# Kernel optimization log

Hardware: AMD Instinct MI355X
Metric: run time of the kernel (lower is better)

Reference implementation:

```python
import jax, jax.numpy as jnp
import numpy as np

B, S, D_IN, E, H = 4, 2048, 1024, 1024, 16
HD = E // H  # 64


def setup_inputs() -> dict:
    key = jax.random.key(0)
    k1, k2, k3, k4, k5 = jax.random.split(key, 5)
    sc_in = 1.0 / np.sqrt(D_IN)
    sc_e = 1.0 / np.sqrt(E)
    return {
        "x": jax.random.normal(k1, (B, S, D_IN), dtype=jnp.float32),
        "w_qkv": jax.random.uniform(k2, (D_IN, 3 * E), dtype=jnp.float32, minval=-sc_in, maxval=sc_in),
        "b_qkv": jax.random.uniform(k3, (3 * E,), dtype=jnp.float32, minval=-sc_in, maxval=sc_in),
        "w_o": jax.random.uniform(k4, (E, E), dtype=jnp.float32, minval=-sc_e, maxval=sc_e),
        "b_o": jax.random.uniform(k5, (E,), dtype=jnp.float32, minval=-sc_e, maxval=sc_e),
    }


def reference(x, w_qkv, b_qkv, w_o, b_o):
    b, s, _ = x.shape
    qkv = x @ w_qkv + b_qkv                          # [B,S,3E]
    qkv = qkv.reshape(b, s, H, 3 * HD)               # [B,S,H,3*HD]
    qkv = qkv.transpose(0, 2, 1, 3)                  # [B,H,S,3*HD]
    q, k, v = jnp.split(qkv, 3, axis=-1)             # each [B,H,S,HD]
    scale = 1.0 / jnp.sqrt(jnp.asarray(HD, dtype=q.dtype))
    logits = jnp.einsum("bhqd,bhkd->bhqk", q, k) * scale
    attn = jax.nn.softmax(logits, axis=-1)
    vals = jnp.einsum("bhqk,bhkd->bhqd", attn, v)    # [B,H,S,HD]
    vals = vals.transpose(0, 2, 1, 3).reshape(b, s, E)
    return vals @ w_o + b_o
```

## Files before the change

### kernel.cpp

```cpp
#include <hip/hip_runtime.h>

typedef __attribute__((ext_vector_type(8))) short bf16x8;
typedef __attribute__((ext_vector_type(4))) float f32x4;
typedef __attribute__((ext_vector_type(16))) float f32x16;
typedef __attribute__((ext_vector_type(4))) unsigned short u16x4;

#define DEV static __device__ __forceinline__

constexpr int Bn = 4, Seq = 2048, DIN = 1024, E = 1024, H = 16, HD = 64;
constexpr int Mrows = Bn * Seq;
constexpr int N3 = 3 * E;

DEV unsigned short f2bf(float f) {
  union { float f; unsigned u; } v; v.f = f;
  return (unsigned short)((v.u + 0x7FFFu + ((v.u >> 16) & 1u)) >> 16);
}

typedef const __attribute__((address_space(1))) unsigned int* gas_p;
typedef __attribute__((address_space(3))) unsigned int* las_p;

DEV void gload_lds16(const void* g, void* l) {
  __builtin_amdgcn_global_load_lds((gas_p)g, (las_p)l, 16, 0, 0);
}

DEV unsigned cvtpk_bf16(float lo, float hi) {
  unsigned r;
  asm("v_cvt_pk_bf16_f32 %0, %1, %2" : "=v"(r) : "v"(lo), "v"(hi));
  return r;
}
DEV float exp2fast(float x) {
  float r;
  asm("v_exp_f32 %0, %1" : "=v"(r) : "v"(x));
  return r;
}
DEV unsigned shx32(unsigned v) { return (unsigned)__shfl_xor((int)v, 32, 64); }
DEV bf16x8 pack4(unsigned w0, unsigned w1, unsigned w2, unsigned w3) {
  union { unsigned u[4]; bf16x8 b; } cv;
  cv.u[0] = w0; cv.u[1] = w1; cv.u[2] = w2; cv.u[3] = w3;
  return cv.b;
}

__global__ void cast_f32_bf16(const float* __restrict__ in,
                              unsigned short* __restrict__ out) {
  size_t i = ((size_t)blockIdx.x * 256 + threadIdx.x) * 8;
  float4 a = *(const float4*)(in + i);
  float4 b = *(const float4*)(in + i + 4);
  union { unsigned short us[8]; bf16x8 v; } r;
  r.us[0] = f2bf(a.x); r.us[1] = f2bf(a.y); r.us[2] = f2bf(a.z); r.us[3] = f2bf(a.w);
  r.us[4] = f2bf(b.x); r.us[5] = f2bf(b.y); r.us[6] = f2bf(b.z); r.us[7] = f2bf(b.w);
  *(bf16x8*)(out + i) = r.v;
}

__global__ void tcast(const float* __restrict__ in, unsigned short* __restrict__ out,
                      int K, int N) {
  __shared__ float tile[64][65];
  int n0 = blockIdx.x * 64, k0 = blockIdx.y * 64;
  int tx = threadIdx.x & 63, ty = threadIdx.x >> 6;
#pragma unroll
  for (int i = 0; i < 64; i += 4)
    tile[ty + i][tx] = in[(size_t)(k0 + ty + i) * N + n0 + tx];
  __syncthreads();
#pragma unroll
  for (int i = 0; i < 64; i += 4)
    out[(size_t)(n0 + ty + i) * K + k0 + tx] = f2bf(tile[tx][ty + i]);
}

template <int EPI, int VOUT>
__global__ __launch_bounds__(256) void gemm_bt(
    const unsigned short* __restrict__ A, const unsigned short* __restrict__ Bt,
    const float* __restrict__ bias, void* __restrict__ Cout,
    unsigned short* __restrict__ vt, int N, int K) {
  constexpr int BM = 128, BN = 128, BK = 32;
  __shared__ alignas(16) unsigned short As[BM * BK];
  __shared__ alignas(16) unsigned short Bs[BN * BK];
  const int tid = threadIdx.x;
  const int wave = tid >> 6, lane = tid & 63;
  const int wr = wave >> 1, wc = wave & 1;
  const int llo = lane & 15, lhi = lane >> 4;
  const int bm = blockIdx.y * BM, bn = blockIdx.x * BN;

  f32x4 acc[4][4] = {};

  for (int kt = 0; kt < K; kt += BK) {
#pragma unroll
    for (int i = 0; i < 2; ++i) {
      int chunk = i * 4 + wave;
      int e = (chunk * 64 + lane) * 8;
      int row = e >> 5, col = e & 31;
      gload_lds16(A + (size_t)(bm + row) * K + kt + col, (char*)As + chunk * 1024);
      gload_lds16(Bt + (size_t)(bn + row) * K + kt + col, (char*)Bs + chunk * 1024);
    }
    __syncthreads();

    bf16x8 af[4], bfr[4];
#pragma unroll
    for (int mt = 0; mt < 4; ++mt)
      af[mt] = *(const bf16x8*)&As[(wr * 64 + mt * 16 + llo) * BK + lhi * 8];
#pragma unroll
    for (int nt = 0; nt < 4; ++nt)
      bfr[nt] = *(const bf16x8*)&Bs[(wc * 64 + nt * 16 + llo) * BK + lhi * 8];
#pragma unroll
    for (int mt = 0; mt < 4; ++mt)
#pragma unroll
      for (int nt = 0; nt < 4; ++nt)
        acc[mt][nt] =
            __builtin_amdgcn_mfma_f32_16x16x32_bf16(af[mt], bfr[nt], acc[mt][nt], 0, 0, 0);
    __syncthreads();
  }

#pragma unroll
  for (int nt = 0; nt < 4; ++nt) {
    int n = bn + wc * 64 + nt * 16 + llo;
    float bv = bias[n];
    if constexpr (VOUT == 1) {
      int h = n / 192, inner = n % 192;
      if (inner < 128) {
        int col = h * 128 + inner;
#pragma unroll
        for (int mt = 0; mt < 4; ++mt)
#pragma unroll
          for (int r = 0; r < 4; ++r) {
            int m = bm + wr * 64 + mt * 16 + lhi * 4 + r;
            ((unsigned short*)Cout)[(size_t)m * 2048 + col] = f2bf(acc[mt][nt][r] + bv);
          }
      } else {
        int d = inner - 128;
#pragma unroll
        for (int mt = 0; mt < 4; ++mt) {
          int m = bm + wr * 64 + mt * 16 + lhi * 4;
          int b = m >> 11, s = m & 2047;
          u16x4 pk;
#pragma unroll
          for (int r = 0; r < 4; ++r) pk[r] = f2bf(acc[mt][nt][r] + bv);
          *(u16x4*)&vt[(size_t)((b * 16 + h) * 64 + d) * Seq + s] = pk;
        }
      }
    } else {
#pragma unroll
      for (int mt = 0; mt < 4; ++mt) {
#pragma unroll
        for (int r = 0; r < 4; ++r) {
          int m = bm + wr * 64 + mt * 16 + lhi * 4 + r;
          float v = acc[mt][nt][r] + bv;
          if constexpr (EPI == 0)
            ((unsigned short*)Cout)[(size_t)m * N + n] = f2bf(v);
          else
            ((float*)Cout)[(size_t)m * N + n] = v;
        }
      }
    }
  }
}

__global__ __launch_bounds__(256) void attn(const unsigned short* __restrict__ qk,
                                            const unsigned short* __restrict__ vt,
                                            unsigned short* __restrict__ O) {
  constexpr int KB = 64, NT = Seq / KB;
  constexpr float SCL = 0.18033688011112042f;
  __shared__ alignas(16) unsigned short Ks[2][64 * 64];
  __shared__ alignas(16) unsigned short Vs[2][64 * 64];
  __shared__ float rbc[4][32];

  const int bh = blockIdx.y, b = bh >> 4, h = bh & 15;
  const int q0 = blockIdx.x * 128;
  const int tid = threadIdx.x, wq = tid >> 6, lane = tid & 63;
  const int lq = lane & 31, hi = lane >> 5;

  const unsigned short* qbase = qk + (size_t)(b * Seq) * 2048 + h * 128;
  const unsigned short* kbase = qbase + 64;
  const unsigned short* vtb = vt + (size_t)bh * 64 * Seq;

  bf16x8 qf[4];
  {
    const unsigned short* qrow = qbase + (size_t)(q0 + wq * 32 + lq) * 2048 + hi * 8;
#pragma unroll
    for (int ds = 0; ds < 4; ++ds) qf[ds] = *(const bf16x8*)(qrow + ds * 16);
  }

  float m = -1e30f, l = 0.f;
  f32x16 oacc[2] = {};

  const int srow = lane >> 3;
  const int scol = ((lane & 7) ^ srow) * 8;

#define STAGE(t, bb)                                                         \
  {                                                                          \
    int kv0 = (t) * KB;                                                      \
    _Pragma("unroll") for (int i = 0; i < 2; ++i) {                          \
      int chunk = i * 4 + wq;                                                \
      int row = chunk * 8 + srow;                                            \
      gload_lds16(kbase + (size_t)(kv0 + row) * 2048 + scol,                 \
                  (char*)&Ks[bb][0] + chunk * 1024);                         \
      gload_lds16(vtb + (size_t)row * Seq + kv0 + scol,                      \
                  (char*)&Vs[bb][0] + chunk * 1024);                         \
    }                                                                        \
  }

#define MKFRAG(dst, s, base)                                                  \
  {                                                                           \
    unsigned a0 = cvtpk_bf16(s[base + 0], s[base + 1]);                       \
    unsigned a1 = cvtpk_bf16(s[base + 2], s[base + 3]);                       \
    unsigned b0 = cvtpk_bf16(s[base + 4], s[base + 5]);                       \
    unsigned b1 = cvtpk_bf16(s[base + 6], s[base + 7]);                       \
    unsigned oa0 = shx32(a0), oa1 = shx32(a1), ob0 = shx32(b0), ob1 = shx32(b1); \
    dst = pack4(hi ? ob0 : a0, hi ? ob1 : a1, hi ? b0 : oa0, hi ? b1 : oa1);  \
  }

  STAGE(0, 0);
  asm volatile("s_waitcnt vmcnt(0)" ::: "memory");
  __syncthreads();

  for (int t = 0; t < NT; ++t) {
    const int bb = t & 1;
    if (t + 1 < NT) STAGE(t + 1, bb ^ 1);

    f32x16 sa0 = {}, sa1 = {};
#pragma unroll
    for (int ds = 0; ds < 4; ++ds) {
      const int ch = 2 * ds + hi;
      bf16x8 k0 = *(const bf16x8*)&Ks[bb][lq * 64 + ((ch ^ (lq & 7)) << 3)];
      bf16x8 k1 = *(const bf16x8*)&Ks[bb][(32 + lq) * 64 + ((ch ^ (lq & 7)) << 3)];
      sa0 = __builtin_amdgcn_mfma_f32_32x32x16_bf16(k0, qf[ds], sa0, 0, 0, 0);
      sa1 = __builtin_amdgcn_mfma_f32_32x32x16_bf16(k1, qf[ds], sa1, 0, 0, 0);
    }

    float tmx[16];
#pragma unroll
    for (int i = 0; i < 16; ++i) tmx[i] = fmaxf(sa0[i], sa1[i]);
#pragma unroll
    for (int st = 8; st > 0; st >>= 1)
#pragma unroll
      for (int i = 0; i < st; ++i) tmx[i] = fmaxf(tmx[i], tmx[i + st]);
    float pmax = tmx[0];
    pmax = fmaxf(pmax, __shfl_xor(pmax, 32, 64));

    float mnew = fmaxf(m, pmax);
    float rfac = exp2fast((m - mnew) * SCL);
    m = mnew;
    float nmc = -m * SCL;

#pragma unroll
    for (int i = 0; i < 16; ++i) sa0[i] = exp2fast(fmaf(sa0[i], SCL, nmc));
#pragma unroll
    for (int i = 0; i < 16; ++i) sa1[i] = exp2fast(fmaf(sa1[i], SCL, nmc));

    float ts[16];
#pragma unroll
    for (int i = 0; i < 16; ++i) ts[i] = sa0[i] + sa1[i];
#pragma unroll
    for (int st = 8; st > 0; st >>= 1)
#pragma unroll
      for (int i = 0; i < st; ++i) ts[i] += ts[i + st];
    float psum = ts[0];
    psum += __shfl_xor(psum, 32, 64);
    l = l * rfac + psum;

    bf16x8 pav[4];
    MKFRAG(pav[0], sa0, 0);
    MKFRAG(pav[1], sa0, 8);
    MKFRAG(pav[2], sa1, 0);
    MKFRAG(pav[3], sa1, 8);

    if (hi == 0) rbc[wq][lq] = rfac;
    f32x4 rf[4];
#pragma unroll
    for (int g = 0; g < 4; ++g) rf[g] = *(const f32x4*)&rbc[wq][g * 8 + hi * 4];
#pragma unroll
    for (int i = 0; i < 16; ++i) {
      float r = rf[i >> 2][i & 3];
      oacc[0][i] *= r;
      oacc[1][i] *= r;
    }

#pragma unroll
    for (int ks = 0; ks < 4; ++ks) {
      const int ch = 2 * ks + hi;
      bf16x8 v0 = *(const bf16x8*)&Vs[bb][lq * 64 + ((ch ^ (lq & 7)) << 3)];
      bf16x8 v1 = *(const bf16x8*)&Vs[bb][(32 + lq) * 64 + ((ch ^ (lq & 7)) << 3)];
      oacc[0] = __builtin_amdgcn_mfma_f32_32x32x16_bf16(pav[ks], v0, oacc[0], 0, 0, 0);
      oacc[1] = __builtin_amdgcn_mfma_f32_32x32x16_bf16(pav[ks], v1, oacc[1], 0, 0, 0);
    }

    asm volatile("s_waitcnt vmcnt(0)" ::: "memory");
    __syncthreads();
  }
#undef STAGE
#undef MKFRAG

  if (hi == 0) rbc[wq][lq] = 1.0f / l;
  f32x4 lf[4];
#pragma unroll
  for (int g = 0; g < 4; ++g) lf[g] = *(const f32x4*)&rbc[wq][g * 8 + hi * 4];
  unsigned short* ob = O + (size_t)(b * Seq + q0 + wq * 32) * E + h * 64 + lq;
#pragma unroll
  for (int db = 0; db < 2; ++db)
#pragma unroll
    for (int i = 0; i < 16; ++i) {
      int ql = (i & 3) + 8 * (i >> 2) + 4 * hi;
      ob[(size_t)ql * E + db * 32] = f2bf(oacc[db][i] * lf[i >> 2][i & 3]);
    }
}

extern "C" void kernel_launch(void* const* d_in, const int* in_sizes, int n_in,
                              void* d_out, int out_size, void* d_ws, size_t ws_size,
                              hipStream_t stream) {
  const float* x = (const float*)d_in[0];
  const float* w_qkv = (const float*)d_in[1];
  const float* b_qkv = (const float*)d_in[2];
  const float* w_o = (const float*)d_in[3];
  const float* b_o = (const float*)d_in[4];
  float* out = (float*)d_out;
  char* ws = (char*)d_ws;

  unsigned short* xb  = (unsigned short*)(ws + 0);
  unsigned short* wqt = (unsigned short*)(ws + 16777216);
  unsigned short* wot = (unsigned short*)(ws + 23068672);
  unsigned short* qkb = (unsigned short*)(ws + 25165824);
  unsigned short* vtb = (unsigned short*)(ws + 58720256);
  unsigned short* atO = (unsigned short*)(ws + 75497472);

  cast_f32_bf16<<<4096, 256, 0, stream>>>(x, xb);
  tcast<<<dim3(48, 16), 256, 0, stream>>>(w_qkv, wqt, DIN, N3);
  tcast<<<dim3(16, 16), 256, 0, stream>>>(w_o, wot, E, E);
  gemm_bt<0, 1><<<dim3(N3 / 128, Mrows / 128), 256, 0, stream>>>(xb, wqt, b_qkv, qkb, vtb, N3, DIN);
  attn<<<dim3(Seq / 128, Bn * H), 256, 0, stream>>>(qkb, vtb, atO);
  gemm_bt<1, 0><<<dim3(E / 128, Mrows / 128), 256, 0, stream>>>(atO, wot, b_o, out, nullptr, E, E);
}
```

Measured before the change: 330.6 us.

## Replace GEMM with 256-row double-buffered XOR-swizzled LDS tiles and 512 threads

Replaces the 128x128x32 GEMM with a 256xBN x64 tile kernel using 8 waves, double-buffered LDS staging via global_load_lds, and an XOR swizzle on LDS columns to avoid bank conflicts. The QKV projection uses BN=192, so each column tile lines up with one head's q/k/v span, and the output projection uses BN=128. The grid is transposed so blockIdx.x walks M. The aim is more data reuse per tile and overlap of global loads with MFMA work. In exchange, register and LDS pressure rise, which may limit occupancy.

Measured after the change: 307.3 us. 1.08x faster.

```diff
diff --git a/kernel.cpp b/kernel.cpp
--- a/kernel.cpp
+++ b/kernel.cpp
@@ -65,69 +65,102 @@
     out[(size_t)(n0 + ty + i) * K + k0 + tx] = f2bf(tile[tx][ty + i]);
 }
 
-template <int EPI, int VOUT>
-__global__ __launch_bounds__(256) void gemm_bt(
+template <int BN, int EPI, int VOUT>
+__global__ __launch_bounds__(512, 2) void gemm256(
     const unsigned short* __restrict__ A, const unsigned short* __restrict__ Bt,
     const float* __restrict__ bias, void* __restrict__ Cout,
     unsigned short* __restrict__ vt, int N, int K) {
-  constexpr int BM = 128, BN = 128, BK = 32;
-  __shared__ alignas(16) unsigned short As[BM * BK];
-  __shared__ alignas(16) unsigned short Bs[BN * BK];
+  constexpr int BM = 256, BK = 64;
+  constexpr int NSPAN = BN / 4;
+  constexpr int NF = NSPAN / 16;
+  constexpr int AC = BM * BK / 8;
+  constexpr int BC = BN * BK / 8;
+  __shared__ alignas(16) unsigned short As[2][BM * BK];
+  __shared__ alignas(16) unsigned short Bs[2][BN * BK];
+
   const int tid = threadIdx.x;
   const int wave = tid >> 6, lane = tid & 63;
-  const int wr = wave >> 1, wc = wave & 1;
+  const int wr = wave >> 2, wc = wave & 3;
   const int llo = lane & 15, lhi = lane >> 4;
-  const int bm = blockIdx.y * BM, bn = blockIdx.x * BN;
-
-  f32x4 acc[4][4] = {};
-
-  for (int kt = 0; kt < K; kt += BK) {
-#pragma unroll
-    for (int i = 0; i < 2; ++i) {
-      int chunk = i * 4 + wave;
-      int e = (chunk * 64 + lane) * 8;
-      int row = e >> 5, col = e & 31;
-      gload_lds16(A + (size_t)(bm + row) * K + kt + col, (char*)As + chunk * 1024);
-      gload_lds16(Bt + (size_t)(bn + row) * K + kt + col, (char*)Bs + chunk * 1024);
-    }
-    __syncthreads();
-
-    bf16x8 af[4], bfr[4];
-#pragma unroll
-    for (int mt = 0; mt < 4; ++mt)
-      af[mt] = *(const bf16x8*)&As[(wr * 64 + mt * 16 + llo) * BK + lhi * 8];
-#pragma unroll
-    for (int nt = 0; nt < 4; ++nt)
-      bfr[nt] = *(const bf16x8*)&Bs[(wc * 64 + nt * 16 + llo) * BK + lhi * 8];
-#pragma unroll
-    for (int mt = 0; mt < 4; ++mt)
-#pragma unroll
-      for (int nt = 0; nt < 4; ++nt)
-        acc[mt][nt] =
-            __builtin_amdgcn_mfma_f32_16x16x32_bf16(af[mt], bfr[nt], acc[mt][nt], 0, 0, 0);
-    __syncthreads();
-  }
-
-#pragma unroll
-  for (int nt = 0; nt < 4; ++nt) {
-    int n = bn + wc * 64 + nt * 16 + llo;
+  const int bm = blockIdx.x * BM, bn = blockIdx.y * BN;
+
+  f32x4 acc[8][NF] = {};
+
+#define GSTAGE(kt, bufi)                                                      \
+  {                                                                           \
+    _Pragma("unroll") for (int i = 0; i < AC / 512; ++i) {                    \
+      int c = i * 512 + tid;                                                  \
+      int row = c >> 3, cs = c & 7;                                           \
+      int col = ((cs ^ (row & 7)) << 3);                                      \
+      gload_lds16(A + (size_t)(bm + row) * K + (kt) + col,                    \
+                  (char*)&As[bufi][0] + c * 16);                              \
+    }                                                                         \
+    _Pragma("unroll") for (int i = 0; i < BC / 512; ++i) {                    \
+      int c = i * 512 + tid;                                                  \
+      int row = c >> 3, cs = c & 7;                                           \
+      int col = ((cs ^ (row & 7)) << 3);                                      \
+      gload_lds16(Bt + (size_t)(bn + row) * K + (kt) + col,                   \
+                  (char*)&Bs[bufi][0] + c * 16);                              \
+    }                                                                         \
+  }
+
+  const int NT = K / BK;
+  GSTAGE(0, 0);
+  asm volatile("s_waitcnt vmcnt(0)" ::: "memory");
+  __syncthreads();
+
+  for (int t = 0; t < NT; ++t) {
+    const int buf = t & 1;
+    if (t + 1 < NT) GSTAGE((t + 1) * BK, buf ^ 1);
+
+#pragma unroll
+    for (int kh = 0; kh < 2; ++kh) {
+      bf16x8 af[8], bfv[NF];
+#pragma unroll
+      for (int mt = 0; mt < 8; ++mt) {
+        int row = wr * 128 + mt * 16 + llo;
+        af[mt] = *(const bf16x8*)&As[buf][row * 64 + (((kh * 4 + lhi) ^ (row & 7)) << 3)];
+      }
+#pragma unroll
+      for (int nt = 0; nt < NF; ++nt) {
+        int row = wc * NSPAN + nt * 16 + llo;
+        bfv[nt] = *(const bf16x8*)&Bs[buf][row * 64 + (((kh * 4 + lhi) ^ (row & 7)) << 3)];
+      }
+#pragma unroll
+      for (int mt = 0; mt < 8; ++mt)
+#pragma unroll
+        for (int nt = 0; nt < NF; ++nt)
+          acc[mt][nt] =
+              __builtin_amdgcn_mfma_f32_16x16x32_bf16(af[mt], bfv[nt], acc[mt][nt], 0, 0, 0);
+    }
+
+    if (t + 1 < NT) {
+      asm volatile("s_waitcnt vmcnt(0)" ::: "memory");
+      __syncthreads();
+    }
+  }
+#undef GSTAGE
+
+#pragma unroll
+  for (int nt = 0; nt < NF; ++nt) {
+    int n = bn + wc * NSPAN + nt * 16 + llo;
     float bv = bias[n];
     if constexpr (VOUT == 1) {
       int h = n / 192, inner = n % 192;
       if (inner < 128) {
         int col = h * 128 + inner;
 #pragma unroll
-        for (int mt = 0; mt < 4; ++mt)
+        for (int mt = 0; mt < 8; ++mt)
 #pragma unroll
           for (int r = 0; r < 4; ++r) {
-            int m = bm + wr * 64 + mt * 16 + lhi * 4 + r;
+            int m = bm + wr * 128 + mt * 16 + lhi * 4 + r;
             ((unsigned short*)Cout)[(size_t)m * 2048 + col] = f2bf(acc[mt][nt][r] + bv);
           }
       } else {
         int d = inner - 128;
 #pragma unroll
-        for (int mt = 0; mt < 4; ++mt) {
-          int m = bm + wr * 64 + mt * 16 + lhi * 4;
+        for (int mt = 0; mt < 8; ++mt) {
+          int m = bm + wr * 128 + mt * 16 + lhi * 4;
           int b = m >> 11, s = m & 2047;
           u16x4 pk;
 #pragma unroll
@@ -137,10 +170,10 @@
       }
     } else {
 #pragma unroll
-      for (int mt = 0; mt < 4; ++mt) {
+      for (int mt = 0; mt < 8; ++mt) {
 #pragma unroll
         for (int r = 0; r < 4; ++r) {
-          int m = bm + wr * 64 + mt * 16 + lhi * 4 + r;
+          int m = bm + wr * 128 + mt * 16 + lhi * 4 + r;
           float v = acc[mt][nt][r] + bv;
           if constexpr (EPI == 0)
             ((unsigned short*)Cout)[(size_t)m * N + n] = f2bf(v);
@@ -322,7 +355,9 @@
   cast_f32_bf16<<<4096, 256, 0, stream>>>(x, xb);
   tcast<<<dim3(48, 16), 256, 0, stream>>>(w_qkv, wqt, DIN, N3);
   tcast<<<dim3(16, 16), 256, 0, stream>>>(w_o, wot, E, E);
-  gemm_bt<0, 1><<<dim3(N3 / 128, Mrows / 128), 256, 0, stream>>>(xb, wqt, b_qkv, qkb, vtb, N3, DIN);
+  gemm256<192, 0, 1><<<dim3(Mrows / 256, N3 / 192), 512, 0, stream>>>(
+      xb, wqt, b_qkv, qkb, vtb, N3, DIN);
   attn<<<dim3(Seq / 128, Bn * H), 256, 0, stream>>>(qkb, vtb, atO);
-  gemm_bt<1, 0><<<dim3(E / 128, Mrows / 128), 256, 0, stream>>>(atO, wot, b_o, out, nullptr, E, E);
-}
+  gemm256<128, 1, 0><<<dim3(Mrows / 256, E / 128), 512, 0, stream>>>(
+      atO, wot, b_o, out, nullptr, E, E);
+}
```
